# Kernel optimization log

Measured on AMD Instinct MI355X. Metric: run time of the kernel, lower is better.

Reference implementation:

```python
import jax, jax.numpy as jnp
import numpy as np

B, S, EMB, H = 2, 2048, 1024, 16
D = EMB // H  # per-head dim = 64
SCALE = 1.0 / np.sqrt(D).astype(np.float32)


def setup_inputs() -> dict:
    key = jax.random.key(0)
    ks = jax.random.split(key, 11)
    lim = 1.0 / np.sqrt(EMB).astype(np.float32)  # torch Linear default init range
    def lin(kw, kb):
        W = jax.random.uniform(kw, (EMB, EMB), jnp.float32, -lim, lim)
        b = jax.random.uniform(kb, (EMB,), jnp.float32, -lim, lim)
        return W, b
    Wq, bq = lin(ks[0], ks[1])
    Wk, bk = lin(ks[2], ks[3])
    Wv, bv = lin(ks[4], ks[5])
    Wo, bo = lin(ks[6], ks[7])
    xq = jax.random.normal(ks[8], (B, S, EMB), jnp.float32)
    xk = jax.random.normal(ks[9], (B, S, EMB), jnp.float32)
    xv = jax.random.normal(ks[10], (B, S, EMB), jnp.float32)
    mask = jnp.tril(jnp.ones((S, S), dtype=jnp.int32))  # causal mask; 0 -> blocked
    return {"xq": xq, "xk": xk, "xv": xv, "mask": mask,
            "Wq": Wq, "bq": bq, "Wk": Wk, "bk": bk,
            "Wv": Wv, "bv": bv, "Wo": Wo, "bo": bo}


def reference(xq, xk, xv, mask, Wq, bq, Wk, bk, Wv, bv, Wo, bo):
    # Projections (torch Linear: x @ W.T + b), then split heads: [B,S,E] -> [B,H,S,D]
    def split_heads(x):
        return x.reshape(B, S, H, D).transpose(0, 2, 1, 3)
    Q = split_heads(xq @ Wq.T + bq)
    K = split_heads(xk @ Wk.T + bk)
    V = split_heads(xv @ Wv.T + bv)
    scores = jnp.einsum("bhqd,bhkd->bhqk", Q, K) * SCALE  # [B,H,S,S]
    scores = jnp.where(mask[None, None, :, :] == 0, jnp.float32(-1e9), scores)
    attn = jax.nn.softmax(scores, axis=-1)  # softmax over key axis (dim=2 per-head in torch)
    res = jnp.einsum("bhqk,bhkd->bhqd", attn, V)
    res = res.transpose(0, 2, 1, 3).reshape(B, S, EMB)  # merge heads back (same slicing layout)
    return res @ Wo.T + bo
```

## Files before the change

### kernel.cpp

```cpp
#include <hip/hip_runtime.h>
#include <hip/hip_bf16.h>

#define BB   2
#define SS   2048
#define EMBD 1024
#define NH   16
#define HD   64
#define SCALE 0.125f
#define NEG_BIG (-1e30f)

typedef __bf16 bf16;
typedef float  floatx4 __attribute__((ext_vector_type(4)));
typedef __bf16 bf16x4  __attribute__((ext_vector_type(4)));
typedef __bf16 bf16x8  __attribute__((ext_vector_type(8)));

typedef const __attribute__((address_space(1))) void* gas_ptr;
typedef __attribute__((address_space(3))) void*       las_ptr;

__device__ __forceinline__ void gl_lds16(const void* g, void* l) {
    __builtin_amdgcn_global_load_lds((gas_ptr)g, (las_ptr)l, 16, 0, 0);
}

__global__ __launch_bounds__(256) void cvt_all(
    const float* __restrict__ xq, const float* __restrict__ xk,
    const float* __restrict__ xv, const float* __restrict__ Wq,
    const float* __restrict__ Wk, const float* __restrict__ Wv,
    const float* __restrict__ Wo, bf16* __restrict__ xqo,
    bf16* __restrict__ xko, bf16* __restrict__ xvo, bf16* __restrict__ Wqo,
    bf16* __restrict__ Wko, bf16* __restrict__ Wvo, bf16* __restrict__ Woo) {
    const int y = blockIdx.y;
    const float* src;
    bf16* dst;
    size_t n;
    const size_t NX = (size_t)BB * SS * EMBD;
    const size_t NW = (size_t)EMBD * EMBD;
    switch (y) {
        case 0: src = xq; dst = xqo; n = NX; break;
        case 1: src = xk; dst = xko; n = NX; break;
        case 2: src = xv; dst = xvo; n = NX; break;
        case 3: src = Wq; dst = Wqo; n = NW; break;
        case 4: src = Wk; dst = Wko; n = NW; break;
        case 5: src = Wv; dst = Wvo; n = NW; break;
        default: src = Wo; dst = Woo; n = NW; break;
    }
    const size_t stride = (size_t)gridDim.x * blockDim.x * 4;
    for (size_t i = ((size_t)blockIdx.x * blockDim.x + threadIdx.x) * 4;
         i < n; i += stride) {
        floatx4 v = *(const floatx4*)(src + i);
        bf16x4 o = {(bf16)v[0], (bf16)v[1], (bf16)v[2], (bf16)v[3]};
        *(bf16x4*)(dst + i) = o;
    }
}

template <int MODE>
__device__ __forceinline__ void gemm_body(const bf16* __restrict__ A,
                                          const bf16* __restrict__ W,
                                          const float* __restrict__ bias,
                                          void* __restrict__ Ov,
                                          int mBase, int nBase) {
    __shared__ __align__(16) bf16 As[128 * 32];
    __shared__ __align__(16) bf16 Bs[128 * 32];

    const int t = threadIdx.x;
    const int l = t & 63, w = t >> 6;
    const int lm = l & 15, lq = l >> 4;
    const int K = 1024;
    const int wm = (w >> 1) * 64, wn = (w & 1) * 64;

    const floatx4 zero = {0.f, 0.f, 0.f, 0.f};
    floatx4 acc[4][4];
#pragma unroll
    for (int i = 0; i < 4; i++)
#pragma unroll
        for (int j = 0; j < 4; j++) acc[i][j] = zero;

    for (int kb = 0; kb < K; kb += 32) {
        __syncthreads();
#pragma unroll
        for (int i = 0; i < 2; i++) {
            int idx  = i * 256 + t;
            int row  = idx >> 2;
            int col  = (idx & 3) * 8;
            const bf16* ga = A + (size_t)(mBase + row) * K + kb + col;
            const bf16* gb = W + (size_t)(nBase + row) * K + kb + col;
            char* la = (char*)As + (i * 256 + w * 64) * 16;
            char* lb = (char*)Bs + (i * 256 + w * 64) * 16;
            gl_lds16(ga, la);
            gl_lds16(gb, lb);
        }
        __syncthreads();

        bf16x8 af[4], bfv[4];
#pragma unroll
        for (int f = 0; f < 4; f++) {
            int rowA = wm + f * 16 + lm;
            af[f] = *(const bf16x8*)&As[rowA * 32 + lq * 8];
            int rowB = wn + f * 16 + lm;
            bfv[f] = *(const bf16x8*)&Bs[rowB * 32 + lq * 8];
        }
        if (MODE == 2) {
#pragma unroll
            for (int i = 0; i < 4; i++)
#pragma unroll
                for (int j = 0; j < 4; j++)
                    acc[i][j] = __builtin_amdgcn_mfma_f32_16x16x32_bf16(
                        bfv[i], af[j], acc[i][j], 0, 0, 0);
        } else {
#pragma unroll
            for (int fm = 0; fm < 4; fm++)
#pragma unroll
                for (int fn = 0; fn < 4; fn++)
                    acc[fm][fn] = __builtin_amdgcn_mfma_f32_16x16x32_bf16(
                        af[fm], bfv[fn], acc[fm][fn], 0, 0, 0);
        }
    }

    if (MODE == 2) {
#pragma unroll
        for (int i = 0; i < 4; i++)
#pragma unroll
            for (int j = 0; j < 4; j++) {
                int m = mBase + wm + j * 16 + lm;
                int b = m >> 11, s = m & 2047;
#pragma unroll
                for (int r = 0; r < 4; r++) {
                    int n = nBase + wn + i * 16 + lq * 4 + r;
                    int h = n >> 6, d = n & 63;
                    float v = acc[i][j][r] + bias[n];
                    ((bf16*)Ov)[((size_t)(b * NH + h) * HD + d) * SS + s] =
                        (bf16)v;
                }
            }
    } else {
#pragma unroll
        for (int fn = 0; fn < 4; fn++) {
            int n = nBase + wn + fn * 16 + lm;
            float bv = bias[n];
#pragma unroll
            for (int fm = 0; fm < 4; fm++) {
                int m0 = mBase + wm + fm * 16 + lq * 4;
#pragma unroll
                for (int r = 0; r < 4; r++) {
                    int m = m0 + r;
                    float v = acc[fm][fn][r] + bv;
                    if (MODE == 0) {
                        int b = m >> 11, s = m & 2047;
                        int h = n >> 6, d = n & 63;
                        ((bf16*)Ov)[(((size_t)(b * NH + h)) * SS + s) * HD +
                                    d] = (bf16)v;
                    } else {
                        ((float*)Ov)[(size_t)m * EMBD + n] = v;
                    }
                }
            }
        }
    }
}

__global__ __launch_bounds__(256, 2) void gemm_qkv(
    const bf16* __restrict__ xq, const bf16* __restrict__ xk,
    const bf16* __restrict__ xv, const bf16* __restrict__ Wq,
    const bf16* __restrict__ Wk, const bf16* __restrict__ Wv,
    const float* __restrict__ bq, const float* __restrict__ bk,
    const float* __restrict__ bv, bf16* __restrict__ Qo,
    bf16* __restrict__ Ko, bf16* __restrict__ Vo) {
    const int z = blockIdx.z;
    if (z == 0)
        gemm_body<0>(xq, Wq, bq, Qo, blockIdx.y * 128, blockIdx.x * 128);
    else if (z == 1)
        gemm_body<0>(xk, Wk, bk, Ko, blockIdx.y * 128, blockIdx.x * 128);
    else
        gemm_body<2>(xv, Wv, bv, Vo, blockIdx.y * 128, blockIdx.x * 128);
}

__global__ __launch_bounds__(256, 2) void gemm_out(
    const bf16* __restrict__ A, const bf16* __restrict__ W,
    const float* __restrict__ bias, float* __restrict__ O) {
    gemm_body<1>(A, W, bias, O, blockIdx.y * 128, blockIdx.x * 128);
}

__global__ __launch_bounds__(256, 2) void attn_fwd(
    const bf16* __restrict__ Qg, const bf16* __restrict__ Kg,
    const bf16* __restrict__ Vtg, bf16* __restrict__ Oatt) {
    __shared__ __align__(16) bf16 Ks[64 * 72];
    __shared__ __align__(16) bf16 VT[64 * 72];
    __shared__ __align__(16) bf16 Ps[4][16 * 72];

    const int t = threadIdx.x;
    const int l = t & 63, w = t >> 6;
    const int lm = l & 15, lq = l >> 4;
    const int qt = (blockIdx.x + blockIdx.y) & 31;
    const int bh = blockIdx.y;
    const size_t kbase = (size_t)bh * SS * HD;
    const size_t vbase = (size_t)bh * HD * SS;

    bf16x8 qa0, qa1;
    {
        const bf16* qp =
            Qg + kbase + (size_t)(qt * 64 + w * 16 + lm) * HD + lq * 8;
        qa0 = *(const bf16x8*)qp;
        qa1 = *(const bf16x8*)(qp + 32);
    }

    const floatx4 zero = {0.f, 0.f, 0.f, 0.f};
    float m_i = NEG_BIG, l_i = 0.f;
    floatx4 od[4];
#pragma unroll
    for (int dt = 0; dt < 4; dt++) od[dt] = zero;

    const int qglob = qt * 64 + w * 16 + lm;

    for (int kt = 0; kt <= qt; ++kt) {
        __syncthreads();
#pragma unroll
        for (int i = 0; i < 2; i++) {
            int idx = i * 256 + t;
            int row = idx >> 3;
            int col = (idx & 7) * 8;
            *(bf16x8*)&Ks[row * 72 + col] = *(const bf16x8*)(
                Kg + kbase + (size_t)(kt * 64 + row) * HD + col);
            *(bf16x8*)&VT[row * 72 + col] = *(const bf16x8*)(
                Vtg + vbase + (size_t)row * SS + kt * 64 + col);
        }
        __syncthreads();

        floatx4 sc[4];
#pragma unroll
        for (int j0 = 0; j0 < 4; j0++) {
            int rowK = j0 * 16 + lm;
            bf16x8 k0 = *(const bf16x8*)&Ks[rowK * 72 + lq * 8];
            bf16x8 k1 = *(const bf16x8*)&Ks[rowK * 72 + 32 + lq * 8];
            floatx4 z = zero;
            z = __builtin_amdgcn_mfma_f32_16x16x32_bf16(k0, qa0, z, 0, 0, 0);
            z = __builtin_amdgcn_mfma_f32_16x16x32_bf16(k1, qa1, z, 0, 0, 0);
            sc[j0] = z;
        }
#pragma unroll
        for (int j0 = 0; j0 < 4; j0++)
#pragma unroll
            for (int r = 0; r < 4; r++) {
                float v = sc[j0][r] * SCALE;
                if (kt == qt) {
                    int key = kt * 64 + j0 * 16 + lq * 4 + r;
                    if (key > qglob) v = NEG_BIG;
                }
                sc[j0][r] = v;
            }
        float mt = sc[0][0];
#pragma unroll
        for (int j0 = 0; j0 < 4; j0++)
#pragma unroll
            for (int r = 0; r < 4; r++) mt = fmaxf(mt, sc[j0][r]);
        mt = fmaxf(mt, __shfl_xor(mt, 16));
        mt = fmaxf(mt, __shfl_xor(mt, 32));
        float mnew = fmaxf(m_i, mt);
        float alpha = __expf(m_i - mnew);
        m_i = mnew;
        float ps = 0.f;
#pragma unroll
        for (int j0 = 0; j0 < 4; j0++)
#pragma unroll
            for (int r = 0; r < 4; r++) {
                float p = __expf(sc[j0][r] - mnew);
                sc[j0][r] = p;
                ps += p;
            }
        ps += __shfl_xor(ps, 16);
        ps += __shfl_xor(ps, 32);
        l_i = l_i * alpha + ps;
#pragma unroll
        for (int j0 = 0; j0 < 4; j0++) {
            bf16x4 pk = {(bf16)sc[j0][0], (bf16)sc[j0][1], (bf16)sc[j0][2],
                         (bf16)sc[j0][3]};
            *(bf16x4*)&Ps[w][lm * 72 + j0 * 16 + lq * 4] = pk;
        }
        float a0 = __shfl(alpha, lq * 4 + 0);
        float a1 = __shfl(alpha, lq * 4 + 1);
        float a2 = __shfl(alpha, lq * 4 + 2);
        float a3 = __shfl(alpha, lq * 4 + 3);
#pragma unroll
        for (int dt = 0; dt < 4; dt++) {
            od[dt][0] *= a0;
            od[dt][1] *= a1;
            od[dt][2] *= a2;
            od[dt][3] *= a3;
        }
        bf16x8 pa0 = *(const bf16x8*)&Ps[w][lm * 72 + lq * 8];
        bf16x8 pa1 = *(const bf16x8*)&Ps[w][lm * 72 + 32 + lq * 8];
#pragma unroll
        for (int dt = 0; dt < 4; dt++) {
            int rowD = dt * 16 + lm;
            bf16x8 v0 = *(const bf16x8*)&VT[rowD * 72 + lq * 8];
            bf16x8 v1 = *(const bf16x8*)&VT[rowD * 72 + 32 + lq * 8];
            od[dt] =
                __builtin_amdgcn_mfma_f32_16x16x32_bf16(pa0, v0, od[dt], 0, 0, 0);
            od[dt] =
                __builtin_amdgcn_mfma_f32_16x16x32_bf16(pa1, v1, od[dt], 0, 0, 0);
        }
    }

    const int b = bh >> 4, h = bh & 15;
    float lr0 = __shfl(l_i, lq * 4 + 0);
    float lr1 = __shfl(l_i, lq * 4 + 1);
    float lr2 = __shfl(l_i, lq * 4 + 2);
    float lr3 = __shfl(l_i, lq * 4 + 3);
#pragma unroll
    for (int dt = 0; dt < 4; dt++) {
        float lr[4] = {lr0, lr1, lr2, lr3};
#pragma unroll
        for (int r = 0; r < 4; r++) {
            int s = qt * 64 + w * 16 + lq * 4 + r;
            float v = od[dt][r] / lr[r];
            Oatt[((size_t)(b * SS + s)) * EMBD + h * HD + dt * 16 + lm] =
                (bf16)v;
        }
    }
}

extern "C" void kernel_launch(void* const* d_in, const int* in_sizes, int n_in,
                              void* d_out, int out_size, void* d_ws,
                              size_t ws_size, hipStream_t stream) {
    const float* xq = (const float*)d_in[0];
    const float* xk = (const float*)d_in[1];
    const float* xv = (const float*)d_in[2];
    const float* Wq = (const float*)d_in[4];
    const float* bq = (const float*)d_in[5];
    const float* Wk = (const float*)d_in[6];
    const float* bk = (const float*)d_in[7];
    const float* Wv = (const float*)d_in[8];
    const float* bv = (const float*)d_in[9];
    const float* Wo = (const float*)d_in[10];
    const float* bo = (const float*)d_in[11];
    float* out = (float*)d_out;

    const size_t NX = (size_t)BB * SS * EMBD;
    const size_t NW = (size_t)EMBD * EMBD;
    bf16* Qw  = (bf16*)d_ws;
    bf16* Kw  = Qw + NX;
    bf16* Vw  = Kw + NX;
    bf16* Aw  = Vw + NX;
    bf16* xqb = Aw + NX;
    bf16* xkb = xqb + NX;
    bf16* xvb = xkb + NX;
    bf16* Wqb = xvb + NX;
    bf16* Wkb = Wqb + NW;
    bf16* Wvb = Wkb + NW;
    bf16* Wob = Wvb + NW;

    cvt_all<<<dim3(1024, 7), 256, 0, stream>>>(xq, xk, xv, Wq, Wk, Wv, Wo,
                                               xqb, xkb, xvb, Wqb, Wkb, Wvb,
                                               Wob);
    gemm_qkv<<<dim3(8, 32, 3), 256, 0, stream>>>(xqb, xkb, xvb, Wqb, Wkb, Wvb,
                                                 bq, bk, bv, Qw, Kw, Vw);
    attn_fwd<<<dim3(SS / 64, BB * NH), 256, 0, stream>>>(Qw, Kw, Vw, Aw);
    gemm_out<<<dim3(8, 32), 256, 0, stream>>>(Aw, Wob, bo, out);
}
```

Before: 249.8 us.

## Pair causal query tiles per block, prefetch K/V into registers, deepen GEMM K-step

```diff
diff --git a/kernel.cpp b/kernel.cpp
--- a/kernel.cpp
+++ b/kernel.cpp
@@ -58,8 +58,8 @@
                                           const float* __restrict__ bias,
                                           void* __restrict__ Ov,
                                           int mBase, int nBase) {
-    __shared__ __align__(16) bf16 As[128 * 32];
-    __shared__ __align__(16) bf16 Bs[128 * 32];
+    __shared__ __align__(16) bf16 As[2 * 128 * 32];
+    __shared__ __align__(16) bf16 Bs[2 * 128 * 32];
 
     const int t = threadIdx.x;
     const int l = t & 63, w = t >> 6;
@@ -74,13 +74,14 @@
 #pragma unroll
         for (int j = 0; j < 4; j++) acc[i][j] = zero;
 
-    for (int kb = 0; kb < K; kb += 32) {
+    for (int kb = 0; kb < K; kb += 64) {
         __syncthreads();
 #pragma unroll
-        for (int i = 0; i < 2; i++) {
-            int idx  = i * 256 + t;
-            int row  = idx >> 2;
-            int col  = (idx & 3) * 8;
+        for (int i = 0; i < 4; i++) {
+            int half = i >> 1;
+            int rem  = (i & 1) * 256 + t;
+            int row  = rem >> 2;
+            int col  = half * 32 + (rem & 3) * 8;
             const bf16* ga = A + (size_t)(mBase + row) * K + kb + col;
             const bf16* gb = W + (size_t)(nBase + row) * K + kb + col;
             char* la = (char*)As + (i * 256 + w * 64) * 16;
@@ -90,28 +91,34 @@
         }
         __syncthreads();
 
-        bf16x8 af[4], bfv[4];
-#pragma unroll
-        for (int f = 0; f < 4; f++) {
-            int rowA = wm + f * 16 + lm;
-            af[f] = *(const bf16x8*)&As[rowA * 32 + lq * 8];
-            int rowB = wn + f * 16 + lm;
-            bfv[f] = *(const bf16x8*)&Bs[rowB * 32 + lq * 8];
-        }
-        if (MODE == 2) {
-#pragma unroll
-            for (int i = 0; i < 4; i++)
-#pragma unroll
-                for (int j = 0; j < 4; j++)
-                    acc[i][j] = __builtin_amdgcn_mfma_f32_16x16x32_bf16(
-                        bfv[i], af[j], acc[i][j], 0, 0, 0);
-        } else {
-#pragma unroll
-            for (int fm = 0; fm < 4; fm++)
-#pragma unroll
-                for (int fn = 0; fn < 4; fn++)
-                    acc[fm][fn] = __builtin_amdgcn_mfma_f32_16x16x32_bf16(
-                        af[fm], bfv[fn], acc[fm][fn], 0, 0, 0);
+#pragma unroll
+        for (int half = 0; half < 2; half++) {
+            const bf16* Ah = As + half * 128 * 32;
+            const bf16* Bh = Bs + half * 128 * 32;
+            bf16x8 af[4], bfv[4];
+#pragma unroll
+            for (int f = 0; f < 4; f++) {
+                int rowA = wm + f * 16 + lm;
+                af[f] = *(const bf16x8*)&Ah[rowA * 32 + lq * 8];
+                int rowB = wn + f * 16 + lm;
+                bfv[f] = *(const bf16x8*)&Bh[rowB * 32 + lq * 8];
+            }
+            if (MODE == 2) {
+#pragma unroll
+                for (int i = 0; i < 4; i++)
+#pragma unroll
+                    for (int j = 0; j < 4; j++)
+                        acc[i][j] = __builtin_amdgcn_mfma_f32_16x16x32_bf16(
+                            bfv[i], af[j], acc[i][j], 0, 0, 0);
+            } else {
+#pragma unroll
+                for (int fm = 0; fm < 4; fm++)
+#pragma unroll
+                    for (int fn = 0; fn < 4; fn++)
+                        acc[fm][fn] =
+                            __builtin_amdgcn_mfma_f32_16x16x32_bf16(
+                                af[fm], bfv[fn], acc[fm][fn], 0, 0, 0);
+            }
         }
     }
 
@@ -189,130 +196,158 @@
     const int t = threadIdx.x;
     const int l = t & 63, w = t >> 6;
     const int lm = l & 15, lq = l >> 4;
-    const int qt = (blockIdx.x + blockIdx.y) & 31;
     const int bh = blockIdx.y;
     const size_t kbase = (size_t)bh * SS * HD;
     const size_t vbase = (size_t)bh * HD * SS;
-
-    bf16x8 qa0, qa1;
-    {
-        const bf16* qp =
-            Qg + kbase + (size_t)(qt * 64 + w * 16 + lm) * HD + lq * 8;
-        qa0 = *(const bf16x8*)qp;
-        qa1 = *(const bf16x8*)(qp + 32);
-    }
-
+    const int b = bh >> 4, h = bh & 15;
     const floatx4 zero = {0.f, 0.f, 0.f, 0.f};
-    float m_i = NEG_BIG, l_i = 0.f;
-    floatx4 od[4];
-#pragma unroll
-    for (int dt = 0; dt < 4; dt++) od[dt] = zero;
-
-    const int qglob = qt * 64 + w * 16 + lm;
-
-    for (int kt = 0; kt <= qt; ++kt) {
-        __syncthreads();
+
+#pragma unroll
+    for (int job = 0; job < 2; ++job) {
+        const int qt = job ? (31 - blockIdx.x) : blockIdx.x;
+
+        bf16x8 qa0, qa1;
+        {
+            const bf16* qp =
+                Qg + kbase + (size_t)(qt * 64 + w * 16 + lm) * HD + lq * 8;
+            qa0 = *(const bf16x8*)qp;
+            qa1 = *(const bf16x8*)(qp + 32);
+        }
+
+        float m_i = NEG_BIG, l_i = 0.f;
+        floatx4 od[4];
+#pragma unroll
+        for (int dt = 0; dt < 4; dt++) od[dt] = zero;
+
+        const int qglob = qt * 64 + w * 16 + lm;
+
+        bf16x8 kreg[2], vreg[2];
 #pragma unroll
         for (int i = 0; i < 2; i++) {
             int idx = i * 256 + t;
             int row = idx >> 3;
             int col = (idx & 7) * 8;
-            *(bf16x8*)&Ks[row * 72 + col] = *(const bf16x8*)(
-                Kg + kbase + (size_t)(kt * 64 + row) * HD + col);
-            *(bf16x8*)&VT[row * 72 + col] = *(const bf16x8*)(
-                Vtg + vbase + (size_t)row * SS + kt * 64 + col);
-        }
-        __syncthreads();
-
-        floatx4 sc[4];
-#pragma unroll
-        for (int j0 = 0; j0 < 4; j0++) {
-            int rowK = j0 * 16 + lm;
-            bf16x8 k0 = *(const bf16x8*)&Ks[rowK * 72 + lq * 8];
-            bf16x8 k1 = *(const bf16x8*)&Ks[rowK * 72 + 32 + lq * 8];
-            floatx4 z = zero;
-            z = __builtin_amdgcn_mfma_f32_16x16x32_bf16(k0, qa0, z, 0, 0, 0);
-            z = __builtin_amdgcn_mfma_f32_16x16x32_bf16(k1, qa1, z, 0, 0, 0);
-            sc[j0] = z;
-        }
-#pragma unroll
-        for (int j0 = 0; j0 < 4; j0++)
+            kreg[i] = *(const bf16x8*)(Kg + kbase + (size_t)row * HD + col);
+            vreg[i] = *(const bf16x8*)(Vtg + vbase + (size_t)row * SS + col);
+        }
+
+        for (int kt = 0; kt <= qt; ++kt) {
+            __syncthreads();
+#pragma unroll
+            for (int i = 0; i < 2; i++) {
+                int idx = i * 256 + t;
+                int row = idx >> 3;
+                int col = (idx & 7) * 8;
+                *(bf16x8*)&Ks[row * 72 + col] = kreg[i];
+                *(bf16x8*)&VT[row * 72 + col] = vreg[i];
+            }
+            __syncthreads();
+            if (kt < qt) {
+#pragma unroll
+                for (int i = 0; i < 2; i++) {
+                    int idx = i * 256 + t;
+                    int row = idx >> 3;
+                    int col = (idx & 7) * 8;
+                    kreg[i] = *(const bf16x8*)(
+                        Kg + kbase + (size_t)((kt + 1) * 64 + row) * HD + col);
+                    vreg[i] = *(const bf16x8*)(
+                        Vtg + vbase + (size_t)row * SS + (kt + 1) * 64 + col);
+                }
+            }
+
+            floatx4 sc[4];
+#pragma unroll
+            for (int j0 = 0; j0 < 4; j0++) {
+                int rowK = j0 * 16 + lm;
+                bf16x8 k0 = *(const bf16x8*)&Ks[rowK * 72 + lq * 8];
+                bf16x8 k1 = *(const bf16x8*)&Ks[rowK * 72 + 32 + lq * 8];
+                floatx4 z = zero;
+                z = __builtin_amdgcn_mfma_f32_16x16x32_bf16(k0, qa0, z, 0, 0,
+                                                            0);
+                z = __builtin_amdgcn_mfma_f32_16x16x32_bf16(k1, qa1, z, 0, 0,
+                                                            0);
+                sc[j0] = z;
+            }
+#pragma unroll
+            for (int j0 = 0; j0 < 4; j0++)
+#pragma unroll
+                for (int r = 0; r < 4; r++) {
+                    float v = sc[j0][r] * SCALE;
+                    if (kt == qt) {
+                        int key = kt * 64 + j0 * 16 + lq * 4 + r;
+                        if (key > qglob) v = NEG_BIG;
+                    }
+                    sc[j0][r] = v;
+                }
+            float mt = sc[0][0];
+#pragma unroll
+            for (int j0 = 0; j0 < 4; j0++)
+#pragma unroll
+                for (int r = 0; r < 4; r++) mt = fmaxf(mt, sc[j0][r]);
+            mt = fmaxf(mt, __shfl_xor(mt, 16));
+            mt = fmaxf(mt, __shfl_xor(mt, 32));
+            float mnew = fmaxf(m_i, mt);
+            float alpha = __expf(m_i - mnew);
+            m_i = mnew;
+            float ps = 0.f;
+#pragma unroll
+            for (int j0 = 0; j0 < 4; j0++)
+#pragma unroll
+                for (int r = 0; r < 4; r++) {
+                    float p = __expf(sc[j0][r] - mnew);
+                    sc[j0][r] = p;
+                    ps += p;
+                }
+            ps += __shfl_xor(ps, 16);
+            ps += __shfl_xor(ps, 32);
+            l_i = l_i * alpha + ps;
+#pragma unroll
+            for (int j0 = 0; j0 < 4; j0++) {
+                bf16x4 pk = {(bf16)sc[j0][0], (bf16)sc[j0][1],
+                             (bf16)sc[j0][2], (bf16)sc[j0][3]};
+                *(bf16x4*)&Ps[w][lm * 72 + j0 * 16 + lq * 4] = pk;
+            }
+            float a0 = __shfl(alpha, lq * 4 + 0);
+            float a1 = __shfl(alpha, lq * 4 + 1);
+            float a2 = __shfl(alpha, lq * 4 + 2);
+            float a3 = __shfl(alpha, lq * 4 + 3);
+#pragma unroll
+            for (int dt = 0; dt < 4; dt++) {
+                od[dt][0] *= a0;
+                od[dt][1] *= a1;
+                od[dt][2] *= a2;
+                od[dt][3] *= a3;
+            }
+            bf16x8 pa0 = *(const bf16x8*)&Ps[w][lm * 72 + lq * 8];
+            bf16x8 pa1 = *(const bf16x8*)&Ps[w][lm * 72 + 32 + lq * 8];
+#pragma unroll
+            for (int dt = 0; dt < 4; dt++) {
+                int rowD = dt * 16 + lm;
+                bf16x8 v0 = *(const bf16x8*)&VT[rowD * 72 + lq * 8];
+                bf16x8 v1 = *(const bf16x8*)&VT[rowD * 72 + 32 + lq * 8];
+                od[dt] = __builtin_amdgcn_mfma_f32_16x16x32_bf16(pa0, v0,
+                                                                 od[dt], 0, 0,
+                                                                 0);
+                od[dt] = __builtin_amdgcn_mfma_f32_16x16x32_bf16(pa1, v1,
+                                                                 od[dt], 0, 0,
+                                                                 0);
+            }
+        }
+
+        float lr0 = __shfl(l_i, lq * 4 + 0);
+        float lr1 = __shfl(l_i, lq * 4 + 1);
+        float lr2 = __shfl(l_i, lq * 4 + 2);
+        float lr3 = __shfl(l_i, lq * 4 + 3);
+        float lr[4] = {lr0, lr1, lr2, lr3};
+#pragma unroll
+        for (int dt = 0; dt < 4; dt++) {
 #pragma unroll
             for (int r = 0; r < 4; r++) {
-                float v = sc[j0][r] * SCALE;
-                if (kt == qt) {
-                    int key = kt * 64 + j0 * 16 + lq * 4 + r;
-                    if (key > qglob) v = NEG_BIG;
-                }
-                sc[j0][r] = v;
-            }
-        float mt = sc[0][0];
-#pragma unroll
-        for (int j0 = 0; j0 < 4; j0++)
-#pragma unroll
-            for (int r = 0; r < 4; r++) mt = fmaxf(mt, sc[j0][r]);
-        mt = fmaxf(mt, __shfl_xor(mt, 16));
-        mt = fmaxf(mt, __shfl_xor(mt, 32));
-        float mnew = fmaxf(m_i, mt);
-        float alpha = __expf(m_i - mnew);
-        m_i = mnew;
-        float ps = 0.f;
-#pragma unroll
-        for (int j0 = 0; j0 < 4; j0++)
-#pragma unroll
-            for (int r = 0; r < 4; r++) {
-                float p = __expf(sc[j0][r] - mnew);
-                sc[j0][r] = p;
-                ps += p;
-            }
-        ps += __shfl_xor(ps, 16);
-        ps += __shfl_xor(ps, 32);
-        l_i = l_i * alpha + ps;
-#pragma unroll
-        for (int j0 = 0; j0 < 4; j0++) {
-            bf16x4 pk = {(bf16)sc[j0][0], (bf16)sc[j0][1], (bf16)sc[j0][2],
-                         (bf16)sc[j0][3]};
-            *(bf16x4*)&Ps[w][lm * 72 + j0 * 16 + lq * 4] = pk;
-        }
-        float a0 = __shfl(alpha, lq * 4 + 0);
-        float a1 = __shfl(alpha, lq * 4 + 1);
-        float a2 = __shfl(alpha, lq * 4 + 2);
-        float a3 = __shfl(alpha, lq * 4 + 3);
-#pragma unroll
-        for (int dt = 0; dt < 4; dt++) {
-            od[dt][0] *= a0;
-            od[dt][1] *= a1;
-            od[dt][2] *= a2;
-            od[dt][3] *= a3;
-        }
-        bf16x8 pa0 = *(const bf16x8*)&Ps[w][lm * 72 + lq * 8];
-        bf16x8 pa1 = *(const bf16x8*)&Ps[w][lm * 72 + 32 + lq * 8];
-#pragma unroll
-        for (int dt = 0; dt < 4; dt++) {
-            int rowD = dt * 16 + lm;
-            bf16x8 v0 = *(const bf16x8*)&VT[rowD * 72 + lq * 8];
-            bf16x8 v1 = *(const bf16x8*)&VT[rowD * 72 + 32 + lq * 8];
-            od[dt] =
-                __builtin_amdgcn_mfma_f32_16x16x32_bf16(pa0, v0, od[dt], 0, 0, 0);
-            od[dt] =
-                __builtin_amdgcn_mfma_f32_16x16x32_bf16(pa1, v1, od[dt], 0, 0, 0);
-        }
-    }
-
-    const int b = bh >> 4, h = bh & 15;
-    float lr0 = __shfl(l_i, lq * 4 + 0);
-    float lr1 = __shfl(l_i, lq * 4 + 1);
-    float lr2 = __shfl(l_i, lq * 4 + 2);
-    float lr3 = __shfl(l_i, lq * 4 + 3);
-#pragma unroll
-    for (int dt = 0; dt < 4; dt++) {
-        float lr[4] = {lr0, lr1, lr2, lr3};
-#pragma unroll
-        for (int r = 0; r < 4; r++) {
-            int s = qt * 64 + w * 16 + lq * 4 + r;
-            float v = od[dt][r] / lr[r];
-            Oatt[((size_t)(b * SS + s)) * EMBD + h * HD + dt * 16 + lm] =
-                (bf16)v;
+                int s = qt * 64 + w * 16 + lq * 4 + r;
+                float v = od[dt][r] / lr[r];
+                Oatt[((size_t)(b * SS + s)) * EMBD + h * HD + dt * 16 + lm] =
+                    (bf16)v;
+            }
         }
     }
 }
@@ -352,6 +387,6 @@
                                                Wob);
     gemm_qkv<<<dim3(8, 32, 3), 256, 0, stream>>>(xqb, xkb, xvb, Wqb, Wkb, Wvb,
                                                  bq, bk, bv, Qw, Kw, Vw);
-    attn_fwd<<<dim3(SS / 64, BB * NH), 256, 0, stream>>>(Qw, Kw, Vw, Aw);
+    attn_fwd<<<dim3(16, BB * NH), 256, 0, stream>>>(Qw, Kw, Vw, Aw);
     gemm_out<<<dim3(8, 32), 256, 0, stream>>>(Aw, Wob, bo, out);
 }
```

Result: faster. 240.2 us (-3.9%).
